# Performance work log

Hardware: AMD Instinct MI355X
Metric: run time of the kernel (lower is better)

## Reference

```python
import jax, jax.numpy as jnp
import numpy as np

N_NODES = 50000

def _spmm(edge_index, edge_weight, feat):
    # adj @ feat where adj is given as COO edge list (dst <- src)
    src = edge_index[1]
    dst = edge_index[0]
    msgs = feat[src] * edge_weight[:, None]  # [E, F]
    return jax.ops.segment_sum(msgs, dst, num_segments=N_NODES)

def setup_inputs() -> dict:
    key = jax.random.key(0)
    ks = jax.random.split(key, 8)
    E = 1600000
    x = jax.random.normal(ks[0], (N_NODES, 512), dtype=jnp.float32)
    edge_index = jax.random.randint(ks[1], (2, E), 0, N_NODES, dtype=jnp.int32)
    edge_weight = jax.random.uniform(ks[2], (E,), dtype=jnp.float32)
    # Glorot-ish init like GraphConvolution.reset_parameters
    W1 = jax.random.normal(ks[3], (512, 128), dtype=jnp.float32) / np.sqrt(512)
    b1 = jax.random.normal(ks[4], (128,), dtype=jnp.float32) * 0.01
    W2 = jax.random.normal(ks[5], (128, 64), dtype=jnp.float32) / np.sqrt(128)
    b2 = jax.random.normal(ks[6], (64,), dtype=jnp.float32) * 0.01
    return {"x": x, "edge_index": edge_index, "edge_weight": edge_weight,
            "W1": W1, "b1": b1, "W2": W2, "b2": b2}

def reference(x, edge_index, edge_weight, W1, b1, W2, b2):
    # eval mode: F.dropout is identity when not training
    # gc1: adj @ (x @ W1) + b1, then relu
    support1 = x @ W1                                   # [N, nhid]
    x1 = jax.nn.relu(_spmm(edge_index, edge_weight, support1) + b1)
    # gc2: adj @ (x1 @ W2) + b2
    support2 = x1 @ W2                                  # [N, out]
    x2 = _spmm(edge_index, edge_weight, support2) + b2
    return (x1, x2)
```

## Files before the change

### kernel.cpp

```cpp
#include <hip/hip_runtime.h>
#include <hip/hip_bf16.h>

#define N_NODES 50000
#define N_EDGES 1600000
#define F_IN    512
#define F_HID   128
#define F_OUT   64
#define NBUK    391
#define EPB     8192
#define CAP     4864

typedef short bf16x8 __attribute__((ext_vector_type(8)));
typedef float f32x4  __attribute__((ext_vector_type(4)));

__device__ __forceinline__ short f32_to_bf16(float f) {
    unsigned u = __float_as_uint(f);
    u += 0x7FFF + ((u >> 16) & 1);
    return (short)(u >> 16);
}
__device__ __forceinline__ float bf16_to_f32(short s) {
    return __uint_as_float(((unsigned)(unsigned short)s) << 16);
}
__device__ __forceinline__ float bf16lo(unsigned u) { return __uint_as_float(u << 16); }
__device__ __forceinline__ float bf16hi(unsigned u) { return __uint_as_float(u & 0xFFFF0000u); }

__device__ __forceinline__ bf16x8 cvt8(float4 lo, float4 hi) {
    union { unsigned u[4]; bf16x8 v; } r;
    asm("v_cvt_pk_bf16_f32 %0, %1, %2" : "=v"(r.u[0]) : "v"(lo.x), "v"(lo.y));
    asm("v_cvt_pk_bf16_f32 %0, %1, %2" : "=v"(r.u[1]) : "v"(lo.z), "v"(lo.w));
    asm("v_cvt_pk_bf16_f32 %0, %1, %2" : "=v"(r.u[2]) : "v"(hi.x), "v"(hi.y));
    asm("v_cvt_pk_bf16_f32 %0, %1, %2" : "=v"(r.u[3]) : "v"(hi.z), "v"(hi.w));
    return r.v;
}


__global__ __launch_bounds__(256) void part_a(const int* __restrict__ dst,
                                              const int* __restrict__ src,
                                              const float* __restrict__ w,
                                              int* __restrict__ gcnt,
                                              uint2* __restrict__ tmp, int E) {
    __shared__ int h[NBUK];
    __shared__ int base[NBUK];
    for (int i = threadIdx.x; i < NBUK; i += 256) h[i] = 0;
    __syncthreads();
    int e0 = blockIdx.x * EPB;
    int e1 = min(e0 + EPB, E);
    for (int e = e0 + threadIdx.x; e < e1; e += 256)
        atomicAdd(&h[dst[e] >> 7], 1);
    __syncthreads();
    for (int i = threadIdx.x; i < NBUK; i += 256) {
        int c = h[i];
        base[i] = c ? atomicAdd(&gcnt[i], c) : 0;
        h[i] = 0;
    }
    __syncthreads();
    for (int e = e0 + threadIdx.x; e < e1; e += 256) {
        int d = dst[e];
        int b = d >> 7;
        int off = base[b] + atomicAdd(&h[b], 1);
        if (off < CAP)
            tmp[(size_t)b * CAP + off] = make_uint2(((unsigned)d << 16) | (unsigned)src[e],
                                                    __float_as_uint(w[e]));
    }
}

__global__ __launch_bounds__(256) void part_b(const uint2* __restrict__ tmp,
                                              const int* __restrict__ gcnt,
                                              int2* __restrict__ rowinfo,
                                              uint2* __restrict__ erec) {
    __shared__ int s[128];
    __shared__ int cur[128];
    int b = blockIdx.x, tid = threadIdx.x;
    int nb0 = b << 7;
    int r0 = b * CAP;
    int cnt_b = min(gcnt[b], CAP);
    int r1 = r0 + cnt_b;
    if (tid < 128) s[tid] = 0;
    __syncthreads();
    for (int i = r0 + tid; i < r1; i += 256)
        atomicAdd(&s[(tmp[i].x >> 16) - nb0], 1);
    __syncthreads();
    int v = (tid < 128) ? s[tid] : 0;
    #pragma unroll
    for (int off = 1; off < 128; off <<= 1) {
        int t = (tid >= off && tid < 128) ? s[tid - off] : 0;
        __syncthreads();
        if (tid < 128) s[tid] += t;
        __syncthreads();
    }
    if (tid < 128) {
        int ex = r0 + s[tid] - v;
        cur[tid] = ex;
        int node = nb0 + tid;
        if (node < N_NODES) rowinfo[node] = make_int2(ex, ex + v);
    }
    __syncthreads();
    for (int i = r0 + tid; i < r1; i += 256) {
        uint2 rec = tmp[i];
        int p = atomicAdd(&cur[(rec.x >> 16) - nb0], 1);
        erec[p] = make_uint2(rec.x & 0xFFFFu, rec.y);
    }
}


template<int KD, int NC>
__global__ void wtrans_frag(const float* __restrict__ W, bf16x8* __restrict__ Bfrag) {
    constexpr int KC = KD / 32, NT = NC / 16;
    int u = blockIdx.x * 256 + threadIdx.x;
    if (u >= KC * NT * 64) return;
    int lane = u & 63;
    int nt   = (u >> 6) % NT;
    int kc   = u / (64 * NT);
    int n = nt * 16 + (lane & 15);
    int k = kc * 32 + (lane >> 4) * 8;
    bf16x8 f;
    #pragma unroll
    for (int j = 0; j < 8; ++j) f[j] = f32_to_bf16(W[(size_t)(k + j) * NC + n]);
    Bfrag[u] = f;
}


template<int NC, int KD>
__global__ __launch_bounds__(256) void mfma_gemm_x(const float* __restrict__ X,
                                                   const bf16x8* __restrict__ Bfrag,
                                                   short* __restrict__ C, int Mt) {
    constexpr int NT = NC / 16, KC = KD / 32;
    constexpr int PFA = (KC < 4) ? KC : 4;
    const int lane = threadIdx.x & 63;
    const int wave = threadIdx.x >> 6;
    const int tile = blockIdx.x * 4 + wave;
    if (tile >= Mt) return;

    const float* xp = X + (size_t)(tile * 16 + (lane & 15)) * KD + ((lane >> 4) * 8);
    const bf16x8* bp = Bfrag + lane;

    f32x4 acc[NT];
    #pragma unroll
    for (int i = 0; i < NT; ++i) acc[i] = (f32x4){0.f, 0.f, 0.f, 0.f};

    float4 alo[PFA], ahi[PFA];
    #pragma unroll
    for (int i = 0; i < PFA; ++i) {
        alo[i] = *(const float4*)(xp + i * 32);
        ahi[i] = *(const float4*)(xp + i * 32 + 4);
    }
    bf16x8 bbuf[NT];
    #pragma unroll
    for (int nt = 0; nt < NT; ++nt) bbuf[nt] = bp[(size_t)nt * 64];

    #pragma unroll
    for (int kc = 0; kc < KC; ++kc) {
        float4 lo = alo[kc % PFA], hi = ahi[kc % PFA];
        int ka = kc + PFA; if (ka > KC - 1) ka = KC - 1;
        alo[kc % PFA] = *(const float4*)(xp + ka * 32);
        ahi[kc % PFA] = *(const float4*)(xp + ka * 32 + 4);
        bf16x8 a = cvt8(lo, hi);
        int kb = (kc + 1 < KC) ? kc + 1 : kc;
        bf16x8 bnew[NT];
        #pragma unroll
        for (int nt = 0; nt < NT; ++nt) {
            bnew[nt] = bp[((size_t)kb * NT + nt) * 64];
            acc[nt] = __builtin_amdgcn_mfma_f32_16x16x32_bf16(a, bbuf[nt], acc[nt], 0, 0, 0);
        }
        #pragma unroll
        for (int nt = 0; nt < NT; ++nt) bbuf[nt] = bnew[nt];
    }

    const int lrow = lane & 15, kgrp = lane >> 4;
    #pragma unroll
    for (int nt = 0; nt < NT; ++nt) {
        #pragma unroll
        for (int r = 0; r < 4; ++r) {
            int grow = tile * 16 + kgrp * 4 + r;
            C[(size_t)grow * NC + nt * 16 + lrow] = f32_to_bf16(acc[nt][r]);
        }
    }
}


template<int NC, int KD>
__global__ __launch_bounds__(256) void mfma_gemm_frag(const bf16x8* __restrict__ Afrag,
                                                      const bf16x8* __restrict__ Bfrag,
                                                      short* __restrict__ C, int Mt) {
    constexpr int NT = NC / 16, KC = KD / 32;
    constexpr int PFA = (KC < 4) ? KC : 4;
    const int lane = threadIdx.x & 63;
    const int wave = threadIdx.x >> 6;
    const int tile = blockIdx.x * 4 + wave;
    if (tile >= Mt) return;

    const bf16x8* ap = Afrag + (size_t)tile * KC * 64 + lane;
    const bf16x8* bp = Bfrag + lane;

    f32x4 acc[NT];
    #pragma unroll
    for (int i = 0; i < NT; ++i) acc[i] = (f32x4){0.f, 0.f, 0.f, 0.f};

    bf16x8 abuf[PFA];
    #pragma unroll
    for (int i = 0; i < PFA; ++i) abuf[i] = ap[(size_t)i * 64];
    bf16x8 bbuf[NT];
    #pragma unroll
    for (int nt = 0; nt < NT; ++nt) bbuf[nt] = bp[(size_t)nt * 64];

    #pragma unroll
    for (int kc = 0; kc < KC; ++kc) {
        bf16x8 a = abuf[kc % PFA];
        int ka = kc + PFA; if (ka > KC - 1) ka = KC - 1;
        abuf[kc % PFA] = ap[(size_t)ka * 64];
        int kb = (kc + 1 < KC) ? kc + 1 : kc;
        bf16x8 bnew[NT];
        #pragma unroll
        for (int nt = 0; nt < NT; ++nt) {
            bnew[nt] = bp[((size_t)kb * NT + nt) * 64];
            acc[nt] = __builtin_amdgcn_mfma_f32_16x16x32_bf16(a, bbuf[nt], acc[nt], 0, 0, 0);
        }
        #pragma unroll
        for (int nt = 0; nt < NT; ++nt) bbuf[nt] = bnew[nt];
    }

    const int lrow = lane & 15, kgrp = lane >> 4;
    #pragma unroll
    for (int nt = 0; nt < NT; ++nt) {
        #pragma unroll
        for (int r = 0; r < 4; ++r) {
            int grow = tile * 16 + kgrp * 4 + r;
            C[(size_t)grow * NC + nt * 16 + lrow] = f32_to_bf16(acc[nt][r]);
        }
    }
}


__global__ __launch_bounds__(64) void spmm128(const int2* __restrict__ rowinfo,
                                              const uint2* __restrict__ erec,
                                              const unsigned* __restrict__ featu,
                                              const float* __restrict__ bias,
                                              float* __restrict__ out,
                                              unsigned* __restrict__ afrag2u) {
    int d = blockIdx.x, tid = threadIdx.x;
    int2 ri = rowinfo[d];
    int beg = ri.x, end = ri.y;
    float a0 = 0.f, a1 = 0.f;
    const unsigned* fp = featu + tid;
    int e = beg;
    if (end - beg >= 8) {
        uint2 r[8];
        #pragma unroll
        for (int j = 0; j < 8; ++j) r[j] = erec[e + j];
        for (; e + 16 <= end; e += 8) {
            unsigned f[8];
            #pragma unroll
            for (int j = 0; j < 8; ++j) f[j] = fp[r[j].x * 64u];
            uint2 rn[8];
            #pragma unroll
            for (int j = 0; j < 8; ++j) rn[j] = erec[e + 8 + j];
            #pragma unroll
            for (int j = 0; j < 8; ++j) {
                float w = __uint_as_float(r[j].y);
                a0 += w * bf16lo(f[j]);
                a1 += w * bf16hi(f[j]);
            }
            #pragma unroll
            for (int j = 0; j < 8; ++j) r[j] = rn[j];
        }
        {
            unsigned f[8];
            #pragma unroll
            for (int j = 0; j < 8; ++j) f[j] = fp[r[j].x * 64u];
            #pragma unroll
            for (int j = 0; j < 8; ++j) {
                float w = __uint_as_float(r[j].y);
                a0 += w * bf16lo(f[j]);
                a1 += w * bf16hi(f[j]);
            }
            e += 8;
        }
    }
    for (; e + 4 <= end; e += 4) {
        uint2 r0 = erec[e], r1 = erec[e + 1], r2 = erec[e + 2], r3 = erec[e + 3];
        unsigned f0 = fp[r0.x * 64u];
        unsigned f1 = fp[r1.x * 64u];
        unsigned f2 = fp[r2.x * 64u];
        unsigned f3 = fp[r3.x * 64u];
        float w0 = __uint_as_float(r0.y), w1 = __uint_as_float(r1.y);
        float w2 = __uint_as_float(r2.y), w3 = __uint_as_float(r3.y);
        a0 += w0 * bf16lo(f0); a1 += w0 * bf16hi(f0);
        a0 += w1 * bf16lo(f1); a1 += w1 * bf16hi(f1);
        a0 += w2 * bf16lo(f2); a1 += w2 * bf16hi(f2);
        a0 += w3 * bf16lo(f3); a1 += w3 * bf16hi(f3);
    }
    for (; e < end; ++e) {
        uint2 r = erec[e];
        unsigned f = fp[r.x * 64u];
        float w = __uint_as_float(r.y);
        a0 += w * bf16lo(f); a1 += w * bf16hi(f);
    }
    float ox = fmaxf(a0 + bias[2 * tid], 0.f);
    float oy = fmaxf(a1 + bias[2 * tid + 1], 0.f);
    *(float2*)&out[(size_t)d * 128 + 2 * tid] = make_float2(ox, oy);
    unsigned packed = (unsigned)(unsigned short)f32_to_bf16(ox) |
                      ((unsigned)(unsigned short)f32_to_bf16(oy) << 16);
    int unit = ((d >> 4) * 4 + (tid >> 4)) * 64 + ((tid >> 2) & 3) * 16 + (d & 15);
    afrag2u[unit * 4 + (tid & 3)] = packed;
}

__global__ __launch_bounds__(64) void spmm64(const int2* __restrict__ rowinfo,
                                             const uint2* __restrict__ erec,
                                             const short* __restrict__ feat,
                                             const float* __restrict__ bias,
                                             float* __restrict__ out) {
    int d = blockIdx.x, tid = threadIdx.x;
    int2 ri = rowinfo[d];
    int beg = ri.x, end = ri.y;
    float acc = 0.f;
    const short* fp = feat + tid;
    int e = beg;
    if (end - beg >= 8) {
        uint2 r[8];
        #pragma unroll
        for (int j = 0; j < 8; ++j) r[j] = erec[e + j];
        for (; e + 16 <= end; e += 8) {
            float f[8];
            #pragma unroll
            for (int j = 0; j < 8; ++j) f[j] = bf16_to_f32(fp[r[j].x * 64u]);
            uint2 rn[8];
            #pragma unroll
            for (int j = 0; j < 8; ++j) rn[j] = erec[e + 8 + j];
            #pragma unroll
            for (int j = 0; j < 8; ++j) acc += __uint_as_float(r[j].y) * f[j];
            #pragma unroll
            for (int j = 0; j < 8; ++j) r[j] = rn[j];
        }
        {
            float f[8];
            #pragma unroll
            for (int j = 0; j < 8; ++j) f[j] = bf16_to_f32(fp[r[j].x * 64u]);
            #pragma unroll
            for (int j = 0; j < 8; ++j) acc += __uint_as_float(r[j].y) * f[j];
            e += 8;
        }
    }
    for (; e + 4 <= end; e += 4) {
        uint2 r0 = erec[e], r1 = erec[e + 1], r2 = erec[e + 2], r3 = erec[e + 3];
        float f0 = bf16_to_f32(fp[r0.x * 64u]);
        float f1 = bf16_to_f32(fp[r1.x * 64u]);
        float f2 = bf16_to_f32(fp[r2.x * 64u]);
        float f3 = bf16_to_f32(fp[r3.x * 64u]);
        acc += __uint_as_float(r0.y) * f0;
        acc += __uint_as_float(r1.y) * f1;
        acc += __uint_as_float(r2.y) * f2;
        acc += __uint_as_float(r3.y) * f3;
    }
    for (; e < end; ++e) {
        uint2 r = erec[e];
        acc += __uint_as_float(r.y) * bf16_to_f32(fp[r.x * 64u]);
    }
    out[(size_t)d * 64 + tid] = acc + bias[tid];
}


extern "C" void kernel_launch(void* const* d_in, const int* in_sizes, int n_in,
                              void* d_out, int out_size, void* d_ws, size_t ws_size,
                              hipStream_t stream) {
    const float* x  = (const float*)d_in[0];
    const int*   ei = (const int*)d_in[1];
    const float* ew = (const float*)d_in[2];
    const float* W1 = (const float*)d_in[3];
    const float* b1 = (const float*)d_in[4];
    const float* W2 = (const float*)d_in[5];
    const float* b2 = (const float*)d_in[6];

    const int* dst = ei;
    const int* src = ei + N_EDGES;

    float* x1 = (float*)d_out;
    float* x2 = x1 + (size_t)N_NODES * F_HID;

    char* ws = (char*)d_ws;
    uint2*  erec     = (uint2*)ws;  ws += (size_t)NBUK * CAP * 8;
    uint2*  tmp      = (uint2*)ws;  ws += (size_t)NBUK * CAP * 8;
    short*  support1 = (short*)ws;  ws += (size_t)N_NODES * F_HID * 2;
    short*  support2 = (short*)ws;  ws += (size_t)N_NODES * F_OUT * 2;
    bf16x8* Afrag2   = (bf16x8*)ws; ws += (size_t)N_NODES * F_HID * 2;
    bf16x8* Bfrag1   = (bf16x8*)ws; ws += (size_t)F_HID * F_IN * 2;
    bf16x8* Bfrag2   = (bf16x8*)ws; ws += (size_t)F_OUT * F_HID * 2;
    int2*   rowinfo  = (int2*)ws;   ws += (size_t)N_NODES * 8;
    int*    gcnt     = (int*)ws;    ws += 400 * 4;

    const int NPB = (N_EDGES + EPB - 1) / EPB;
    const int MT  = N_NODES / 16;

    hipMemsetAsync(gcnt, 0, NBUK * sizeof(int), stream);
    part_a<<<NPB, 256, 0, stream>>>(dst, src, ew, gcnt, tmp, N_EDGES);
    part_b<<<NBUK, 256, 0, stream>>>(tmp, gcnt, rowinfo, erec);

    wtrans_frag<F_IN, F_HID><<<32, 256, 0, stream>>>(W1, Bfrag1);
    wtrans_frag<F_HID, F_OUT><<<4, 256, 0, stream>>>(W2, Bfrag2);

    mfma_gemm_x<F_HID, F_IN><<<(MT + 3) / 4, 256, 0, stream>>>(x, Bfrag1, support1, MT);

    spmm128<<<N_NODES, 64, 0, stream>>>(rowinfo, erec, (const unsigned*)support1, b1, x1,
                                        (unsigned*)Afrag2);

    mfma_gemm_frag<F_OUT, F_HID><<<(MT + 3) / 4, 256, 0, stream>>>(Afrag2, Bfrag2, support2, MT);

    spmm64<<<N_NODES, 64, 0, stream>>>(rowinfo, erec, support2, b2, x2);
}
```

Measured before the change: 355.1 us.

## Keep W1 fragments register-resident and split N across waves in first GEMM

The x@W1 GEMM is restructured so each wave owns a 32-column slice of the output (two 16-wide tiles) and holds all of its B fragments for the full K in registers, then loops over four consecutive 16-row M tiles. This removes repeated B-fragment loads per tile and amortizes them across tiles. The four waves in a block share the same M tiles but cover different N slices, so the X rows are read by four waves (through cache). The large register array (32 bf16x8) may lower occupancy.

```diff
diff --git a/kernel.cpp b/kernel.cpp
--- a/kernel.cpp
+++ b/kernel.cpp
@@ -120,59 +120,67 @@
 }
 
 
-template<int NC, int KD>
-__global__ __launch_bounds__(256) void mfma_gemm_x(const float* __restrict__ X,
-                                                   const bf16x8* __restrict__ Bfrag,
-                                                   short* __restrict__ C, int Mt) {
-    constexpr int NT = NC / 16, KC = KD / 32;
+template<int NC, int KD, int NTS, int MLOOP>
+__global__ __launch_bounds__(256) void mfma_gemm_xr(const float* __restrict__ X,
+                                                    const bf16x8* __restrict__ Bfrag,
+                                                    short* __restrict__ C, int Mt) {
+    constexpr int KC  = KD / 32;
+    constexpr int NT  = NC / 16;
+    constexpr int NSL = NT / NTS;
+    constexpr int MW  = 4 / NSL;
     constexpr int PFA = (KC < 4) ? KC : 4;
     const int lane = threadIdx.x & 63;
     const int wave = threadIdx.x >> 6;
-    const int tile = blockIdx.x * 4 + wave;
-    if (tile >= Mt) return;
-
-    const float* xp = X + (size_t)(tile * 16 + (lane & 15)) * KD + ((lane >> 4) * 8);
-    const bf16x8* bp = Bfrag + lane;
-
-    f32x4 acc[NT];
-    #pragma unroll
-    for (int i = 0; i < NT; ++i) acc[i] = (f32x4){0.f, 0.f, 0.f, 0.f};
-
-    float4 alo[PFA], ahi[PFA];
-    #pragma unroll
-    for (int i = 0; i < PFA; ++i) {
-        alo[i] = *(const float4*)(xp + i * 32);
-        ahi[i] = *(const float4*)(xp + i * 32 + 4);
-    }
-    bf16x8 bbuf[NT];
-    #pragma unroll
-    for (int nt = 0; nt < NT; ++nt) bbuf[nt] = bp[(size_t)nt * 64];
-
-    #pragma unroll
-    for (int kc = 0; kc < KC; ++kc) {
-        float4 lo = alo[kc % PFA], hi = ahi[kc % PFA];
-        int ka = kc + PFA; if (ka > KC - 1) ka = KC - 1;
-        alo[kc % PFA] = *(const float4*)(xp + ka * 32);
-        ahi[kc % PFA] = *(const float4*)(xp + ka * 32 + 4);
-        bf16x8 a = cvt8(lo, hi);
-        int kb = (kc + 1 < KC) ? kc + 1 : kc;
-        bf16x8 bnew[NT];
-        #pragma unroll
-        for (int nt = 0; nt < NT; ++nt) {
-            bnew[nt] = bp[((size_t)kb * NT + nt) * 64];
-            acc[nt] = __builtin_amdgcn_mfma_f32_16x16x32_bf16(a, bbuf[nt], acc[nt], 0, 0, 0);
-        }
-        #pragma unroll
-        for (int nt = 0; nt < NT; ++nt) bbuf[nt] = bnew[nt];
-    }
-
-    const int lrow = lane & 15, kgrp = lane >> 4;
-    #pragma unroll
-    for (int nt = 0; nt < NT; ++nt) {
-        #pragma unroll
-        for (int r = 0; r < 4; ++r) {
-            int grow = tile * 16 + kgrp * 4 + r;
-            C[(size_t)grow * NC + nt * 16 + lrow] = f32_to_bf16(acc[nt][r]);
+    const int ws   = wave % NSL;
+    const int wm   = wave / NSL;
+    const int m0   = (blockIdx.x * MW + wm) * MLOOP;
+
+    bf16x8 breg[KC * NTS];
+    #pragma unroll
+    for (int kc = 0; kc < KC; ++kc)
+        #pragma unroll
+        for (int nt = 0; nt < NTS; ++nt)
+            breg[kc * NTS + nt] = Bfrag[((size_t)kc * NT + ws * NTS + nt) * 64 + lane];
+
+    const int r_lo = lane & 15;
+    const int cg   = lane >> 4;
+
+    for (int ml = 0; ml < MLOOP; ++ml) {
+        int tile = m0 + ml;
+        if (tile >= Mt) return;
+        const float* xp = X + (size_t)(tile * 16 + r_lo) * KD + cg * 8;
+
+        f32x4 acc[NTS];
+        #pragma unroll
+        for (int i = 0; i < NTS; ++i) acc[i] = (f32x4){0.f, 0.f, 0.f, 0.f};
+
+        float4 alo[PFA], ahi[PFA];
+        #pragma unroll
+        for (int i = 0; i < PFA; ++i) {
+            alo[i] = *(const float4*)(xp + i * 32);
+            ahi[i] = *(const float4*)(xp + i * 32 + 4);
+        }
+
+        #pragma unroll
+        for (int kc = 0; kc < KC; ++kc) {
+            float4 lo = alo[kc % PFA], hi = ahi[kc % PFA];
+            int ka = kc + PFA; if (ka > KC - 1) ka = KC - 1;
+            alo[kc % PFA] = *(const float4*)(xp + ka * 32);
+            ahi[kc % PFA] = *(const float4*)(xp + ka * 32 + 4);
+            bf16x8 a = cvt8(lo, hi);
+            #pragma unroll
+            for (int nt = 0; nt < NTS; ++nt)
+                acc[nt] = __builtin_amdgcn_mfma_f32_16x16x32_bf16(a, breg[kc * NTS + nt],
+                                                                  acc[nt], 0, 0, 0);
+        }
+
+        #pragma unroll
+        for (int nt = 0; nt < NTS; ++nt) {
+            #pragma unroll
+            for (int r = 0; r < 4; ++r) {
+                int grow = tile * 16 + cg * 4 + r;
+                C[(size_t)grow * NC + (ws * NTS + nt) * 16 + r_lo] = f32_to_bf16(acc[nt][r]);
+            }
         }
     }
 }
@@ -397,7 +405,11 @@
     wtrans_frag<F_IN, F_HID><<<32, 256, 0, stream>>>(W1, Bfrag1);
     wtrans_frag<F_HID, F_OUT><<<4, 256, 0, stream>>>(W2, Bfrag2);
 
-    mfma_gemm_x<F_HID, F_IN><<<(MT + 3) / 4, 256, 0, stream>>>(x, Bfrag1, support1, MT);
+    {
+        constexpr int MLOOP = 4;
+        int blocks = (MT + MLOOP - 1) / MLOOP;
+        mfma_gemm_xr<F_HID, F_IN, 2, MLOOP><<<blocks, 256, 0, stream>>>(x, Bfrag1, support1, MT);
+    }
 
     spmm128<<<N_NODES, 64, 0, stream>>>(rowinfo, erec, (const unsigned*)support1, b1, x1,
                                         (unsigned*)Afrag2);
```

After: 380.3 us. 7.1% more time.

## Replace first GEMM with LDS double-buffered 64x128 block tile

Applied to the files above, without the earlier changes.

The x@W1 GEMM previously had each wave compute a full 16x128 strip, loading the B fragments straight from global memory. It now uses a 64-row block tile. A and B chunks are staged through double-buffered shared memory with register prefetch, and the four waves split the tile 2x2 so each B fragment load is shared across more rows. This targets global and L2 traffic for the weights and aims to overlap loads with MFMA work, at the cost of two barriers per K step and extra LDS use.

```diff
diff --git a/kernel.cpp b/kernel.cpp
--- a/kernel.cpp
+++ b/kernel.cpp
@@ -119,60 +119,95 @@
     Bfrag[u] = f;
 }
 
-
-template<int NC, int KD>
-__global__ __launch_bounds__(256) void mfma_gemm_x(const float* __restrict__ X,
-                                                   const bf16x8* __restrict__ Bfrag,
-                                                   short* __restrict__ C, int Mt) {
-    constexpr int NT = NC / 16, KC = KD / 32;
-    constexpr int PFA = (KC < 4) ? KC : 4;
-    const int lane = threadIdx.x & 63;
-    const int wave = threadIdx.x >> 6;
-    const int tile = blockIdx.x * 4 + wave;
-    if (tile >= Mt) return;
-
-    const float* xp = X + (size_t)(tile * 16 + (lane & 15)) * KD + ((lane >> 4) * 8);
-    const bf16x8* bp = Bfrag + lane;
-
-    f32x4 acc[NT];
-    #pragma unroll
-    for (int i = 0; i < NT; ++i) acc[i] = (f32x4){0.f, 0.f, 0.f, 0.f};
-
-    float4 alo[PFA], ahi[PFA];
-    #pragma unroll
-    for (int i = 0; i < PFA; ++i) {
-        alo[i] = *(const float4*)(xp + i * 32);
-        ahi[i] = *(const float4*)(xp + i * 32 + 4);
-    }
-    bf16x8 bbuf[NT];
-    #pragma unroll
-    for (int nt = 0; nt < NT; ++nt) bbuf[nt] = bp[(size_t)nt * 64];
-
-    #pragma unroll
-    for (int kc = 0; kc < KC; ++kc) {
-        float4 lo = alo[kc % PFA], hi = ahi[kc % PFA];
-        int ka = kc + PFA; if (ka > KC - 1) ka = KC - 1;
-        alo[kc % PFA] = *(const float4*)(xp + ka * 32);
-        ahi[kc % PFA] = *(const float4*)(xp + ka * 32 + 4);
-        bf16x8 a = cvt8(lo, hi);
-        int kb = (kc + 1 < KC) ? kc + 1 : kc;
-        bf16x8 bnew[NT];
-        #pragma unroll
-        for (int nt = 0; nt < NT; ++nt) {
-            bnew[nt] = bp[((size_t)kb * NT + nt) * 64];
-            acc[nt] = __builtin_amdgcn_mfma_f32_16x16x32_bf16(a, bbuf[nt], acc[nt], 0, 0, 0);
-        }
-        #pragma unroll
-        for (int nt = 0; nt < NT; ++nt) bbuf[nt] = bnew[nt];
-    }
-
-    const int lrow = lane & 15, kgrp = lane >> 4;
-    #pragma unroll
-    for (int nt = 0; nt < NT; ++nt) {
-        #pragma unroll
-        for (int r = 0; r < 4; ++r) {
-            int grow = tile * 16 + kgrp * 4 + r;
-            C[(size_t)grow * NC + nt * 16 + lrow] = f32_to_bf16(acc[nt][r]);
+template<int KD , int NC >
+__global__ __launch_bounds__(256) void mfma_gemm_s1(const float* __restrict__ X,
+                                                    const bf16x8* __restrict__ Bfrag,
+                                                    short* __restrict__ C, int Mrows) {
+    constexpr int S = KD / 32;
+    __shared__ char lds[2][16384];
+    const int tid  = threadIdx.x;
+    const int lane = tid & 63;
+    const int wave = tid >> 6;
+    const int wm = wave >> 1, wn = wave & 1;
+    const int B0 = blockIdx.x * 64;
+    const int r_lo = lane & 15, cg = lane >> 4;
+
+    int rowA = B0 + wave * 16 + r_lo;
+    if (rowA > Mrows - 1) rowA = Mrows - 1;
+    const char* gA = (const char*)(X + (size_t)rowA * KD) + cg * 32;
+    const char* gB = (const char*)Bfrag + (size_t)(wave * 2) * 1024 + (size_t)lane * 16;
+
+    const int ldsA0 = (0 * 256 + wave * 64 + lane) * 16;
+    const int ldsA1 = (1 * 256 + wave * 64 + lane) * 16;
+    const int ldsB0 = 8192 + (wave * 2 + 0) * 1024 + lane * 16;
+    const int ldsB1 = 8192 + (wave * 2 + 1) * 1024 + lane * 16;
+
+    f32x4 acc[2][4];
+    #pragma unroll
+    for (int m = 0; m < 2; ++m)
+        #pragma unroll
+        for (int n = 0; n < 4; ++n) acc[m][n] = (f32x4){0.f, 0.f, 0.f, 0.f};
+
+    float4 ra0 = *(const float4*)(gA);
+    float4 ra1 = *(const float4*)(gA + 16);
+    float4 rb0 = *(const float4*)(gB);
+    float4 rb1 = *(const float4*)(gB + 1024);
+    *(float4*)(&lds[0][ldsA0]) = ra0;
+    *(float4*)(&lds[0][ldsA1]) = ra1;
+    *(float4*)(&lds[0][ldsB0]) = rb0;
+    *(float4*)(&lds[0][ldsB1]) = rb1;
+    __syncthreads();
+
+    int buf = 0;
+    for (int s = 0; s < S; ++s) {
+        if (s + 1 < S) {
+            size_t oa = (size_t)(s + 1) * 128;
+            size_t ob = (size_t)(s + 1) * 8192;
+            ra0 = *(const float4*)(gA + oa);
+            ra1 = *(const float4*)(gA + 16 + oa);
+            rb0 = *(const float4*)(gB + ob);
+            rb1 = *(const float4*)(gB + 1024 + ob);
+        }
+        const char* A_ = lds[buf];
+        const char* B_ = lds[buf] + 8192;
+        bf16x8 bb[4];
+        #pragma unroll
+        for (int n = 0; n < 4; ++n)
+            bb[n] = *(const bf16x8*)(B_ + (wn * 4 + n) * 1024 + lane * 16);
+        #pragma unroll
+        for (int m = 0; m < 2; ++m) {
+            int t = wm * 2 + m;
+            float4 lo = *(const float4*)(A_ + (0 * 256 + t * 64 + lane) * 16);
+            float4 hi = *(const float4*)(A_ + (1 * 256 + t * 64 + lane) * 16);
+            bf16x8 a = cvt8(lo, hi);
+            #pragma unroll
+            for (int n = 0; n < 4; ++n)
+                acc[m][n] = __builtin_amdgcn_mfma_f32_16x16x32_bf16(a, bb[n], acc[m][n], 0, 0, 0);
+        }
+        if (s + 1 < S) {
+            __syncthreads();
+            char* An = lds[buf ^ 1];
+            *(float4*)(&An[ldsA0]) = ra0;
+            *(float4*)(&An[ldsA1]) = ra1;
+            *(float4*)(&An[ldsB0]) = rb0;
+            *(float4*)(&An[ldsB1]) = rb1;
+            __syncthreads();
+            buf ^= 1;
+        }
+    }
+
+    #pragma unroll
+    for (int m = 0; m < 2; ++m) {
+        int tile16 = (B0 >> 4) + wm * 2 + m;
+        if (tile16 * 16 < Mrows) {
+            #pragma unroll
+            for (int n = 0; n < 4; ++n) {
+                #pragma unroll
+                for (int r = 0; r < 4; ++r) {
+                    int grow = tile16 * 16 + cg * 4 + r;
+                    C[(size_t)grow * NC + (wn * 4 + n) * 16 + r_lo] = f32_to_bf16(acc[m][n][r]);
+                }
+            }
         }
     }
 }
@@ -397,7 +432,10 @@
     wtrans_frag<F_IN, F_HID><<<32, 256, 0, stream>>>(W1, Bfrag1);
     wtrans_frag<F_HID, F_OUT><<<4, 256, 0, stream>>>(W2, Bfrag2);
 
-    mfma_gemm_x<F_HID, F_IN><<<(MT + 3) / 4, 256, 0, stream>>>(x, Bfrag1, support1, MT);
+    {
+        int blocks = (N_NODES + 63) / 64;
+        mfma_gemm_s1<F_IN, F_HID><<<blocks, 256, 0, stream>>>(x, Bfrag1, support1, N_NODES);
+    }
 
     spmm128<<<N_NODES, 64, 0, stream>>>(rowinfo, erec, (const unsigned*)support1, b1, x1,
                                         (unsigned*)Afrag2);
```

After: 353.0 us. Within noise of the previous version (-0.6%).
